# Optimization experiments

Hardware: AMD Instinct MI355X
Metric: run time of the kernel (lower is better)

The kernel has to match this reference:

```python
import jax, jax.numpy as jnp
import numpy as np

D = 1024       # d_model
DR = 1024      # d_rec
FFN = 4096     # ffn_inner
K = 4          # conv_kernel
B, T = 2, 4096
CHUNK = 64
EPS = 1e-6


def setup_inputs() -> dict:
    key = jax.random.key(0)
    ks = jax.random.split(key, 8)
    s = lambda k, shape, scale: jax.random.normal(k, shape, jnp.float32) * scale
    db = np.zeros((DR,), np.float32)
    q = DR // 4
    db[:q] = -2.2
    db[q:3 * q] = 0.0
    db[3 * q:] = 4.6
    return {
        "x": s(ks[0], (B, T, D), 1.0),
        "pre_norm_w": jnp.ones((D,), jnp.float32),
        "conv_w": s(ks[1], (D, 1, K), 0.3),
        "conv_b": jnp.zeros((D,), jnp.float32),
        "w_a": s(ks[2], (DR, D), 0.02),
        "w_i": s(ks[3], (DR, D), 0.02),
        "w_v": s(ks[4], (DR, D), 0.02),
        "out_proj_w": s(ks[5], (D, DR), 0.02),
        "decay_bias": jnp.asarray(db),
        "ffn_norm_w": jnp.ones((D,), jnp.float32),
        "w_gate_up": s(ks[6], (2 * FFN, D), 0.02),
        "w_down": s(ks[7], (D, FFN), 0.02),
    }


def rmsnorm(x, w):
    return x * jax.lax.rsqrt(jnp.mean(x * x, axis=-1, keepdims=True) + EPS) * w


def lin(x, w):  # nn.Linear weight layout (out, in)
    return jnp.einsum('btd,od->bto', x, w)


def causal_conv(h, w, b):
    # depthwise causal conv: h (B,T,D), w (D,1,K)
    hc = jnp.transpose(h, (0, 2, 1))  # (B,D,T)
    out = jax.lax.conv_general_dilated(
        hc, w, window_strides=(1,), padding=[(K - 1, 0)],
        dimension_numbers=('NCH', 'OIH', 'NCH'), feature_group_count=D)
    return jnp.transpose(out, (0, 2, 1)) + b


def chunked_scan(a, v):
    b, s, d = a.shape
    pad = (-s) % CHUNK
    af = jnp.pad(a, ((0, 0), (0, pad), (0, 0)), constant_values=1.0)
    vf = jnp.pad(v, ((0, 0), (0, pad), (0, 0)))
    n = (s + pad) // CHUNK
    dc = af.reshape(b, n, CHUNK, d)
    vc = vf.reshape(b, n, CHUNK, d)
    cum_decay = jnp.exp(jnp.cumsum(jnp.log(jnp.clip(dc, 1e-10)), axis=2))
    intra = cum_decay * jnp.cumsum(vc / jnp.clip(cum_decay, 1e-10), axis=2)

    def step(state, xs):
        cd, it = xs  # (B,CHUNK,d) each
        cs = it + cd * state[:, None, :]
        return cs[:, -1], cs

    _, states = jax.lax.scan(
        step, jnp.zeros((b, d), jnp.float32),
        (jnp.transpose(cum_decay, (1, 0, 2, 3)), jnp.transpose(intra, (1, 0, 2, 3))))
    return jnp.transpose(states, (1, 0, 2, 3)).reshape(b, n * CHUNK, d)[:, :s]


def reference(x, pre_norm_w, conv_w, conv_b, w_a, w_i, w_v, out_proj_w,
              decay_bias, ffn_norm_w, w_gate_up, w_down):
    h = rmsnorm(x, pre_norm_w)
    h = causal_conv(h, conv_w, conv_b)
    a = jax.nn.sigmoid(lin(h, w_a) + decay_bias)
    i_gate = jax.nn.sigmoid(lin(h, w_i))
    v = lin(h, w_v)
    input_signal = jnp.sqrt(jnp.clip(1.0 - a * a, 1e-8)) * (i_gate * v)
    rec_out = chunked_scan(a, input_signal).astype(x.dtype)
    x = x + lin(rec_out, out_proj_w)
    hn = rmsnorm(x, ffn_norm_w)
    gu = lin(hn, w_gate_up)
    gate, up = gu[..., :FFN], gu[..., FFN:]
    x = x + lin(jax.nn.silu(gate) * up, w_down)
    return x
```

## Files before the change

kernel.cpp:

```cpp
#include <hip/hip_runtime.h>

typedef __bf16 bf16_t;
typedef bf16_t bf16x4 __attribute__((ext_vector_type(4)));
typedef bf16_t bf16x8 __attribute__((ext_vector_type(8)));
typedef float f32x4 __attribute__((ext_vector_type(4)));

#define DD 1024
#define TT 4096

__device__ __forceinline__ void gload16(const void* g, void* l) {
    __builtin_amdgcn_global_load_lds(
        (const __attribute__((address_space(1))) void*)g,
        (__attribute__((address_space(3))) void*)l, 16, 0, 0);
}

__global__ __launch_bounds__(256) void cvt_bf16_k(const float* __restrict__ s,
                                                  bf16_t* __restrict__ d, int n) {
    int i = (blockIdx.x * 256 + threadIdx.x) * 4;
    if (i < n) {
        const float4 v = *(const float4*)(s + i);
        bf16x4 o;
        o[0] = (bf16_t)v.x; o[1] = (bf16_t)v.y; o[2] = (bf16_t)v.z; o[3] = (bf16_t)v.w;
        *(bf16x4*)(d + i) = o;
    }
}

__global__ __launch_bounds__(256) void cvt_ileave_k(const float* __restrict__ s0,
                                                    const float* __restrict__ s1,
                                                    bf16_t* __restrict__ d, int total) {
    int i = (blockIdx.x * 256 + threadIdx.x) * 4;
    if (i < total) {
        const int rp = i >> 10, k = i & 1023;
        const int c = rp >> 1;
        const float* src = ((rp & 1) ? s1 : s0) + (long)c * 1024 + k;
        const float4 v = *(const float4*)src;
        bf16x4 o;
        o[0] = (bf16_t)v.x; o[1] = (bf16_t)v.y; o[2] = (bf16_t)v.z; o[3] = (bf16_t)v.w;
        *(bf16x4*)(d + i) = o;
    }
}

__global__ __launch_bounds__(256) void rmsnorm_k(const float* __restrict__ x,
                                                 const float* __restrict__ w,
                                                 bf16_t* __restrict__ ob) {
    const long row = blockIdx.x;
    const float* xr = x + row * DD;
    const int t4 = threadIdx.x * 4;
    float4 v = *(const float4*)(xr + t4);
    float s = v.x*v.x + v.y*v.y + v.z*v.z + v.w*v.w;
    #pragma unroll
    for (int off = 1; off < 64; off <<= 1) s += __shfl_xor(s, off);
    __shared__ float red[4];
    if ((threadIdx.x & 63) == 0) red[threadIdx.x >> 6] = s;
    __syncthreads();
    float tot = red[0] + red[1] + red[2] + red[3];
    float sc = rsqrtf(tot * (1.0f / DD) + 1e-6f);
    float4 wv = *(const float4*)(w + t4);
    bf16x4 o;
    o[0] = (bf16_t)(v.x*sc*wv.x); o[1] = (bf16_t)(v.y*sc*wv.y);
    o[2] = (bf16_t)(v.z*sc*wv.z); o[3] = (bf16_t)(v.w*sc*wv.w);
    *(bf16x4*)(ob + row * DD + t4) = o;
}

__global__ __launch_bounds__(256) void conv_k(const bf16_t* __restrict__ h,
                                              const float* __restrict__ cw,
                                              const float* __restrict__ cb,
                                              bf16_t* __restrict__ hc) {
    const long idx = (long)blockIdx.x * 256 + threadIdx.x;
    const int d = (int)(idx & (DD - 1));
    const long bt = idx >> 10;
    const int t = (int)(bt & (TT - 1));
    const float w0 = cw[d*4+0], w1 = cw[d*4+1], w2 = cw[d*4+2], w3 = cw[d*4+3];
    const bf16_t* hp = h + bt * DD + d;
    float acc = cb[d] + (float)hp[0] * w3;
    if (t >= 1) acc += (float)hp[-DD]     * w2;
    if (t >= 2) acc += (float)hp[-2*DD]   * w1;
    if (t >= 3) acc += (float)hp[-3*DD]   * w0;
    hc[idx] = (bf16_t)acc;
}

__global__ __launch_bounds__(256) void scan1_k(const float* __restrict__ ap,
                                               const float* __restrict__ sp,
                                               float* __restrict__ cd63,
                                               float* __restrict__ i63) {
    const int d = blockIdx.x * 256 + threadIdx.x;
    const int c = blockIdx.y;
    const int b = blockIdx.z;
    const long rowbase = (long)b * TT + (long)c * 64;
    float la = 0.0f, rs = 0.0f, cdv = 0.0f, it = 0.0f;
    for (int t = 0; t < 64; t++) {
        const long off = (rowbase + t) * DD + d;
        const float a = ap[off];
        const float s = sp[off];
        const float sig = sqrtf(fmaxf(1.0f - a * a, 1e-8f)) * s;
        la += __logf(fmaxf(a, 1e-10f));
        cdv = __expf(la);
        rs += sig / fmaxf(cdv, 1e-10f);
        it = cdv * rs;
    }
    const long o = ((long)b * 64 + c) * DD + d;
    cd63[o] = cdv;
    i63[o]  = it;
}

__global__ __launch_bounds__(256) void scan2_k(const float* __restrict__ cd63,
                                               const float* __restrict__ i63,
                                               float* __restrict__ carry_in) {
    const int g = blockIdx.x * 256 + threadIdx.x;
    const int b = g >> 10, d = g & (DD - 1);
    float st = 0.0f;
    for (int c = 0; c < 64; c++) {
        const long o = ((long)b * 64 + c) * DD + d;
        carry_in[o] = st;
        st = i63[o] + cd63[o] * st;
    }
}

__global__ __launch_bounds__(256) void scan3_k(const float* __restrict__ ap,
                                               const float* __restrict__ sp,
                                               const float* __restrict__ carry_in,
                                               bf16_t* __restrict__ rec) {
    const int d = blockIdx.x * 256 + threadIdx.x;
    const int c = blockIdx.y;
    const int b = blockIdx.z;
    const long rowbase = (long)b * TT + (long)c * 64;
    const float carry = carry_in[((long)b * 64 + c) * DD + d];
    float la = 0.0f, rs = 0.0f;
    for (int t = 0; t < 64; t++) {
        const long off = (rowbase + t) * DD + d;
        const float a = ap[off];
        const float s = sp[off];
        const float sig = sqrtf(fmaxf(1.0f - a * a, 1e-8f)) * s;
        la += __logf(fmaxf(a, 1e-10f));
        const float cdv = __expf(la);
        rs += sig / fmaxf(cdv, 1e-10f);
        rec[off] = (bf16_t)(cdv * rs + cdv * carry);
    }
}

enum { EPI_SIGB = 0, EPI_ADDRES = 1, EPI_IV = 2, EPI_GU = 3 };

template<int EPI, int NREP>
__global__ __launch_bounds__(512, 2) void gemm8p_k(const bf16_t* __restrict__ Ag,
                                                   const bf16_t* __restrict__ Bg,
                                                   int M, int N, int K,
                                                   float* outF, bf16_t* outB,
                                                   const float* aux, int ldc) {
    constexpr int BN  = NREP * 64;
    constexpr int ASZ = 16384;
    constexpr int BSZ = BN * 64;
    constexpr int BUF = ASZ + BSZ;
    extern __shared__ bf16_t smem[];
    const int tid = threadIdx.x;
    const int l = tid & 63;
    const int w = tid >> 6;
    const int wm = w >> 2, wn = w & 3;

    const int gx = gridDim.x;
    const int gy = gridDim.y;
    const int lin = blockIdx.y * gx + blockIdx.x;
    long row0, col0;
    if ((gy & 7) == 0) {
        const int rpc = gy >> 3;
        const int q = lin >> 3;
        row0 = (long)((lin & 7) * rpc + q % rpc) * 256;
        col0 = (long)(q / rpc) * (long)BN;
    } else {
        row0 = (long)blockIdx.y * 256;
        col0 = (long)blockIdx.x * BN;
    }

    const int srow = l >> 3;
    const int scol = ((l & 7) ^ srow) * 8;
    const long aBase = row0 + srow;
    const long bBase = col0 + srow;
    const int R0a = w * 32;
    const int R0b = w * (BN / 8);

    const int NT = K >> 6;
    f32x4 acc[8][NREP] = {};

    #pragma unroll
    for (int i = 0; i < NREP; i++)
        gload16(Bg + (bBase + R0b + i * 8) * (long)K + scol, &smem[ASZ + (R0b + i * 8) * 64]);
    #pragma unroll
    for (int i = 0; i < 4; i++)
        gload16(Ag + (aBase + R0a + i * 8) * (long)K + scol, &smem[(R0a + i * 8) * 64]);
    #pragma unroll
    for (int i = 0; i < NREP; i++)
        gload16(Bg + (bBase + R0b + i * 8) * (long)K + 64 + scol, &smem[BUF + ASZ + (R0b + i * 8) * 64]);

    const int lq = (l >> 4) * 8;
    const int rA = wm * 128 + (l & 15);
    const int rB = wn * (NREP * 16) + (l & 15);

    for (int t = 0; t < NT; t++) {
        const int cb = (t & 1) * BUF;
        const int ob = BUF - cb;
        const long kg1 = (long)(t + 1) * 64 + scol;
        const long kg2 = (long)(t + 2) * 64 + scol;
        bf16x8 Bf[2][NREP], Af[4];

        if (t + 1 < NT) {
            gload16(Ag + (aBase + R0a) * (long)K + kg1, &smem[ob + R0a * 64]);
            gload16(Ag + (aBase + R0a + 8) * (long)K + kg1, &smem[ob + (R0a + 8) * 64]);
        }
        if (t == NT - 1)            { asm volatile("s_waitcnt vmcnt(0)" ::: "memory"); }
        else if constexpr (NREP == 4) { asm volatile("s_waitcnt vmcnt(6)" ::: "memory"); }
        else                        { asm volatile("s_waitcnt vmcnt(4)" ::: "memory"); }
        asm volatile("s_barrier" ::: "memory");
        #pragma unroll
        for (int n = 0; n < NREP; n++) {
            const int r = rB + n * 16;
            Bf[0][n] = *(const bf16x8*)&smem[cb + ASZ + r * 64 + (((lq * 2) ^ ((r & 7) << 4)) >> 1)];
        }
        #pragma unroll
        for (int m = 0; m < 4; m++) {
            const int r = rA + m * 16;
            Af[m] = *(const bf16x8*)&smem[cb + r * 64 + (((lq * 2) ^ ((r & 7) << 4)) >> 1)];
        }
        __builtin_amdgcn_s_setprio(1);
        #pragma unroll
        for (int m = 0; m < 4; m++)
            #pragma unroll
            for (int n = 0; n < NREP; n++)
                acc[m][n] = __builtin_amdgcn_mfma_f32_16x16x32_bf16(Af[m], Bf[0][n], acc[m][n], 0, 0, 0);
        __builtin_amdgcn_s_setprio(0);
        asm volatile("s_barrier" ::: "memory");

        #pragma unroll
        for (int m = 0; m < 4; m++) {
            const int r = rA + 64 + m * 16;
            Af[m] = *(const bf16x8*)&smem[cb + r * 64 + (((lq * 2) ^ ((r & 7) << 4)) >> 1)];
        }
        #pragma unroll
        for (int n = 0; n < NREP; n++) {
            const int r = rB + n * 16;
            Bf[1][n] = *(const bf16x8*)&smem[cb + ASZ + r * 64 + ((((lq * 2) ^ ((r & 7) << 4)) ^ 64) >> 1)];
        }
        if (t + 1 < NT) {
            gload16(Ag + (aBase + R0a + 16) * (long)K + kg1, &smem[ob + (R0a + 16) * 64]);
            gload16(Ag + (aBase + R0a + 24) * (long)K + kg1, &smem[ob + (R0a + 24) * 64]);
        }
        asm volatile("s_barrier" ::: "memory");
        __builtin_amdgcn_s_setprio(1);
        #pragma unroll
        for (int m = 0; m < 4; m++)
            #pragma unroll
            for (int n = 0; n < NREP; n++)
                acc[m + 4][n] = __builtin_amdgcn_mfma_f32_16x16x32_bf16(Af[m], Bf[0][n], acc[m + 4][n], 0, 0, 0);
        __builtin_amdgcn_s_setprio(0);
        asm volatile("s_barrier" ::: "memory");

        #pragma unroll
        for (int m = 0; m < 4; m++) {
            const int r = rA + m * 16;
            Af[m] = *(const bf16x8*)&smem[cb + r * 64 + ((((lq + 32) * 2) ^ ((r & 7) << 4)) >> 1)];
        }
        if (t + 2 < NT) {
            gload16(Bg + (bBase + R0b) * (long)K + kg2, &smem[cb + ASZ + R0b * 64]);
            if constexpr (NREP == 4)
                gload16(Bg + (bBase + R0b + 8) * (long)K + kg2, &smem[cb + ASZ + (R0b + 8) * 64]);
        }
        asm volatile("s_barrier" ::: "memory");
        __builtin_amdgcn_s_setprio(1);
        #pragma unroll
        for (int m = 0; m < 4; m++)
            #pragma unroll
            for (int n = 0; n < NREP; n++)
                acc[m][n] = __builtin_amdgcn_mfma_f32_16x16x32_bf16(Af[m], Bf[1][n], acc[m][n], 0, 0, 0);
        __builtin_amdgcn_s_setprio(0);
        asm volatile("s_barrier" ::: "memory");

        #pragma unroll
        for (int m = 0; m < 4; m++) {
            const int r = rA + 64 + m * 16;
            Af[m] = *(const bf16x8*)&smem[cb + r * 64 + ((((lq + 32) * 2) ^ ((r & 7) << 4)) >> 1)];
        }
        if (t + 2 < NT) {
            if constexpr (NREP == 4) {
                gload16(Bg + (bBase + R0b + 16) * (long)K + kg2, &smem[cb + ASZ + (R0b + 16) * 64]);
                gload16(Bg + (bBase + R0b + 24) * (long)K + kg2, &smem[cb + ASZ + (R0b + 24) * 64]);
            } else {
                gload16(Bg + (bBase + R0b + 8) * (long)K + kg2, &smem[cb + ASZ + (R0b + 8) * 64]);
            }
        }
        asm volatile("s_barrier" ::: "memory");
        __builtin_amdgcn_s_setprio(1);
        #pragma unroll
        for (int m = 0; m < 4; m++)
            #pragma unroll
            for (int n = 0; n < NREP; n++)
                acc[m + 4][n] = __builtin_amdgcn_mfma_f32_16x16x32_bf16(Af[m], Bf[1][n], acc[m + 4][n], 0, 0, 0);
        __builtin_amdgcn_s_setprio(0);
        asm volatile("s_barrier" ::: "memory");
    }

    #pragma unroll
    for (int m = 0; m < 8; m++) {
        const long r0 = row0 + wm * 128 + m * 16 + (l >> 4) * 4;
        #pragma unroll
        for (int n = 0; n < NREP; n++) {
            const long cc = col0 + wn * (NREP * 16) + n * 16 + (l & 15);
            f32x4 v = acc[m][n];
            #pragma unroll
            for (int j = 0; j < 4; j++) {
                const long r = r0 + j;
                const float xv = v[j];
                if (EPI == EPI_SIGB) {
                    outF[r * ldc + cc] = 1.0f / (1.0f + __expf(-(xv + aux[cc])));
                } else if (EPI == EPI_ADDRES) {
                    outF[r * ldc + cc] = xv + aux[r * ldc + cc];
                } else if (EPI == EPI_IV) {
                    const float px = __shfl_xor(xv, 1);
                    if ((l & 1) == 0)
                        outF[r * ldc + (cc >> 1)] = px / (1.0f + __expf(-xv));
                } else {
                    const float px = __shfl_xor(xv, 1);
                    if ((l & 1) == 0)
                        outB[r * ldc + (cc >> 1)] = (bf16_t)(xv / (1.0f + __expf(-xv)) * px);
                }
            }
        }
    }
}

extern "C" void kernel_launch(void* const* d_in, const int* in_sizes, int n_in,
                              void* d_out, int out_size, void* d_ws, size_t ws_size,
                              hipStream_t stream) {
    const float* x   = (const float*)d_in[0];
    const float* pnw = (const float*)d_in[1];
    const float* cw  = (const float*)d_in[2];
    const float* cb  = (const float*)d_in[3];
    const float* wa  = (const float*)d_in[4];
    const float* wi  = (const float*)d_in[5];
    const float* wv  = (const float*)d_in[6];
    const float* wop = (const float*)d_in[7];
    const float* db  = (const float*)d_in[8];
    const float* fnw = (const float*)d_in[9];
    const float* wgu = (const float*)d_in[10];
    const float* wdn = (const float*)d_in[11];
    float* out = (float*)d_out;

    char* ws = (char*)d_ws;
    bf16_t* wab   = (bf16_t*)(ws + 0);
    bf16_t* wivb  = (bf16_t*)(ws + 2097152);
    bf16_t* wopb  = (bf16_t*)(ws + 6291456);
    bf16_t* wgub  = (bf16_t*)(ws + 8388608);
    bf16_t* wdnb  = (bf16_t*)(ws + 25165824);
    bf16_t* hb    = (bf16_t*)(ws + 33554432);
    bf16_t* hn    = hb;
    bf16_t* hc    = (bf16_t*)(ws + 50331648);
    bf16_t* rec   = hc;
    float*  a_p   = (float*)(ws + 67108864);
    float*  s_p   = (float*)(ws + 100663296);
    bf16_t* act   = (bf16_t*)(ws + 67108864);
    float*  cd63  = (float*)(ws + 134217728);
    float*  i63   = (float*)(ws + 134742016);
    float*  carry = (float*)(ws + 135266304);

    const int LDS4 = 131072;
    const int LDS2 = 98304;
    hipFuncSetAttribute((const void*)gemm8p_k<EPI_SIGB, 2>,   hipFuncAttributeMaxDynamicSharedMemorySize, LDS2);
    hipFuncSetAttribute((const void*)gemm8p_k<EPI_IV, 4>,     hipFuncAttributeMaxDynamicSharedMemorySize, LDS4);
    hipFuncSetAttribute((const void*)gemm8p_k<EPI_ADDRES, 2>, hipFuncAttributeMaxDynamicSharedMemorySize, LDS2);
    hipFuncSetAttribute((const void*)gemm8p_k<EPI_GU, 4>,     hipFuncAttributeMaxDynamicSharedMemorySize, LDS4);

    cvt_bf16_k  <<<1024, 256, 0, stream>>>(wa,  wab,  1048576);
    cvt_ileave_k<<<2048, 256, 0, stream>>>(wi,  wv, wivb, 2097152);
    cvt_bf16_k  <<<1024, 256, 0, stream>>>(wop, wopb, 1048576);
    cvt_ileave_k<<<8192, 256, 0, stream>>>(wgu, wgu + 4194304, wgub, 8388608);
    cvt_bf16_k  <<<4096, 256, 0, stream>>>(wdn, wdnb, 4194304);

    rmsnorm_k<<<8192, 256, 0, stream>>>(x, pnw, hb);
    conv_k<<<32768, 256, 0, stream>>>(hb, cw, cb, hc);

    gemm8p_k<EPI_SIGB, 2><<<dim3(8, 32), 512, LDS2, stream>>>(hc, wab,  8192, 1024, 1024,
                                                              a_p, nullptr, db, 1024);
    gemm8p_k<EPI_IV, 4>  <<<dim3(8, 32), 512, LDS4, stream>>>(hc, wivb, 8192, 2048, 1024,
                                                              s_p, nullptr, nullptr, 1024);
    scan1_k<<<dim3(4, 64, 2), 256, 0, stream>>>(a_p, s_p, cd63, i63);
    scan2_k<<<8, 256, 0, stream>>>(cd63, i63, carry);
    scan3_k<<<dim3(4, 64, 2), 256, 0, stream>>>(a_p, s_p, carry, rec);

    gemm8p_k<EPI_ADDRES, 2><<<dim3(8, 32), 512, LDS2, stream>>>(rec, wopb, 8192, 1024, 1024,
                                                                out, nullptr, x, 1024);
    rmsnorm_k<<<8192, 256, 0, stream>>>(out, fnw, hn);
    gemm8p_k<EPI_GU, 4><<<dim3(32, 32), 512, LDS4, stream>>>(hn, wgub, 8192, 8192, 1024,
                                                             nullptr, act, nullptr, 4096);
    gemm8p_k<EPI_ADDRES, 2><<<dim3(8, 32), 512, LDS2, stream>>>(act, wdnb, 8192, 1024, 4096,
                                                                out, nullptr, out, 1024);
}
```

Baseline: 480.8 us.

## Restructure GEMM main loop into two-phase schedule with full-tile prefetch

Replaces the eight-phase GEMM inner loop, which interleaved partial global-to-LDS loads with four MFMA groups and many barriers, with a two-phase loop. Each iteration issues whole next-next tile loads at once, preloads the A and B fragments for both k-halves into registers, and uses two barriers per iteration instead of eight. The aim is to cut barrier and synchronisation overhead and give longer uninterrupted MFMA runs. The cost is higher register pressure from holding more fragments, and bursty global-load issue that may hide latency less well.

After: 468.8 us. 1.03x faster.

```diff
diff --git a/kernel.cpp b/kernel.cpp
--- a/kernel.cpp
+++ b/kernel.cpp
@@ -141,7 +141,7 @@
 enum { EPI_SIGB = 0, EPI_ADDRES = 1, EPI_IV = 2, EPI_GU = 3 };
 
 template<int EPI, int NREP>
-__global__ __launch_bounds__(512, 2) void gemm8p_k(const bf16_t* __restrict__ Ag,
+__global__ __launch_bounds__(512, 2) void gemm2p_k(const bf16_t* __restrict__ Ag,
                                                    const bf16_t* __restrict__ Bg,
                                                    int M, int N, int K,
                                                    float* outF, bf16_t* outB,
@@ -180,121 +180,98 @@
     const int NT = K >> 6;
     f32x4 acc[8][NREP] = {};
 
-    #pragma unroll
-    for (int i = 0; i < NREP; i++)
-        gload16(Bg + (bBase + R0b + i * 8) * (long)K + scol, &smem[ASZ + (R0b + i * 8) * 64]);
-    #pragma unroll
-    for (int i = 0; i < 4; i++)
-        gload16(Ag + (aBase + R0a + i * 8) * (long)K + scol, &smem[(R0a + i * 8) * 64]);
-    #pragma unroll
-    for (int i = 0; i < NREP; i++)
-        gload16(Bg + (bBase + R0b + i * 8) * (long)K + 64 + scol, &smem[BUF + ASZ + (R0b + i * 8) * 64]);
-
-    const int lq = (l >> 4) * 8;
+    const int lq2 = (l >> 4) * 16;
     const int rA = wm * 128 + (l & 15);
     const int rB = wn * (NREP * 16) + (l & 15);
+    const int eA0 = rA * 64 + ((lq2 ^ ((rA & 7) << 4)) >> 1);
+    const int eB0 = ASZ + rB * 64 + ((lq2 ^ ((rB & 7) << 4)) >> 1);
+
+    #define STAGE_A(tt, off)                                                          \
+        { const long kgk = (long)(tt) * 64 + scol;                                    \
+          _Pragma("unroll")                                                           \
+          for (int i = 0; i < 4; i++)                                                 \
+              gload16(Ag + (aBase + R0a + i * 8) * (long)K + kgk,                     \
+                      &smem[(off) + (R0a + i * 8) * 64]); }
+    #define STAGE_B(tt, off)                                                          \
+        { const long kgk = (long)(tt) * 64 + scol;                                    \
+          _Pragma("unroll")                                                           \
+          for (int i = 0; i < NREP; i++)                                              \
+              gload16(Bg + (bBase + R0b + i * 8) * (long)K + kgk,                     \
+                      &smem[(off) + ASZ + (R0b + i * 8) * 64]); }
+
+    STAGE_A(0, 0); STAGE_B(0, 0);
+    STAGE_A(1, BUF); STAGE_B(1, BUF);
+    if constexpr (NREP == 4) { asm volatile("s_waitcnt vmcnt(8)" ::: "memory"); }
+    else                     { asm volatile("s_waitcnt vmcnt(6)" ::: "memory"); }
+    asm volatile("s_barrier" ::: "memory");
+
+    bf16x8 pA[2][4], pB[2][NREP];
+    #pragma unroll
+    for (int kk = 0; kk < 2; kk++) {
+        const int xo = kk * 32;
+        #pragma unroll
+        for (int n = 0; n < NREP; n++)
+            pB[kk][n] = *(const bf16x8*)&smem[(eB0 ^ xo) + n * 1024];
+        #pragma unroll
+        for (int m = 0; m < 4; m++)
+            pA[kk][m] = *(const bf16x8*)&smem[(eA0 ^ xo) + m * 1024];
+    }
 
     for (int t = 0; t < NT; t++) {
-        const int cb = (t & 1) * BUF;
-        const int ob = BUF - cb;
-        const long kg1 = (long)(t + 1) * 64 + scol;
-        const long kg2 = (long)(t + 2) * 64 + scol;
-        bf16x8 Bf[2][NREP], Af[4];
-
-        if (t + 1 < NT) {
-            gload16(Ag + (aBase + R0a) * (long)K + kg1, &smem[ob + R0a * 64]);
-            gload16(Ag + (aBase + R0a + 8) * (long)K + kg1, &smem[ob + (R0a + 8) * 64]);
-        }
-        if (t == NT - 1)            { asm volatile("s_waitcnt vmcnt(0)" ::: "memory"); }
-        else if constexpr (NREP == 4) { asm volatile("s_waitcnt vmcnt(6)" ::: "memory"); }
-        else                        { asm volatile("s_waitcnt vmcnt(4)" ::: "memory"); }
-        asm volatile("s_barrier" ::: "memory");
-        #pragma unroll
-        for (int n = 0; n < NREP; n++) {
-            const int r = rB + n * 16;
-            Bf[0][n] = *(const bf16x8*)&smem[cb + ASZ + r * 64 + (((lq * 2) ^ ((r & 7) << 4)) >> 1)];
-        }
-        #pragma unroll
-        for (int m = 0; m < 4; m++) {
-            const int r = rA + m * 16;
-            Af[m] = *(const bf16x8*)&smem[cb + r * 64 + (((lq * 2) ^ ((r & 7) << 4)) >> 1)];
-        }
+        const int co = (t & 1) ? BUF : 0;
+        const int oo = BUF - co;
+        bf16x8 a1[2][4];
+
         __builtin_amdgcn_s_setprio(1);
         #pragma unroll
-        for (int m = 0; m < 4; m++)
-            #pragma unroll
-            for (int n = 0; n < NREP; n++)
-                acc[m][n] = __builtin_amdgcn_mfma_f32_16x16x32_bf16(Af[m], Bf[0][n], acc[m][n], 0, 0, 0);
+        for (int kk = 0; kk < 2; kk++)
+            #pragma unroll
+            for (int m = 0; m < 4; m++)
+                #pragma unroll
+                for (int n = 0; n < NREP; n++)
+                    acc[m][n] = __builtin_amdgcn_mfma_f32_16x16x32_bf16(pA[kk][m], pB[kk][n], acc[m][n], 0, 0, 0);
         __builtin_amdgcn_s_setprio(0);
-        asm volatile("s_barrier" ::: "memory");
-
-        #pragma unroll
-        for (int m = 0; m < 4; m++) {
-            const int r = rA + 64 + m * 16;
-            Af[m] = *(const bf16x8*)&smem[cb + r * 64 + (((lq * 2) ^ ((r & 7) << 4)) >> 1)];
-        }
-        #pragma unroll
-        for (int n = 0; n < NREP; n++) {
-            const int r = rB + n * 16;
-            Bf[1][n] = *(const bf16x8*)&smem[cb + ASZ + r * 64 + ((((lq * 2) ^ ((r & 7) << 4)) ^ 64) >> 1)];
-        }
-        if (t + 1 < NT) {
-            gload16(Ag + (aBase + R0a + 16) * (long)K + kg1, &smem[ob + (R0a + 16) * 64]);
-            gload16(Ag + (aBase + R0a + 24) * (long)K + kg1, &smem[ob + (R0a + 24) * 64]);
+        #pragma unroll
+        for (int kk = 0; kk < 2; kk++) {
+            const int xo = kk * 32;
+            #pragma unroll
+            for (int m = 0; m < 4; m++)
+                a1[kk][m] = *(const bf16x8*)&smem[co + (eA0 ^ xo) + 4096 + m * 1024];
         }
         asm volatile("s_barrier" ::: "memory");
+
+        if (t + 2 < NT) { STAGE_A(t + 2, co); STAGE_B(t + 2, co); }
         __builtin_amdgcn_s_setprio(1);
         #pragma unroll
-        for (int m = 0; m < 4; m++)
-            #pragma unroll
-            for (int n = 0; n < NREP; n++)
-                acc[m + 4][n] = __builtin_amdgcn_mfma_f32_16x16x32_bf16(Af[m], Bf[0][n], acc[m + 4][n], 0, 0, 0);
+        for (int kk = 0; kk < 2; kk++)
+            #pragma unroll
+            for (int m = 0; m < 4; m++)
+                #pragma unroll
+                for (int n = 0; n < NREP; n++)
+                    acc[m + 4][n] = __builtin_amdgcn_mfma_f32_16x16x32_bf16(a1[kk][m], pB[kk][n], acc[m + 4][n], 0, 0, 0);
         __builtin_amdgcn_s_setprio(0);
-        asm volatile("s_barrier" ::: "memory");
-
-        #pragma unroll
-        for (int m = 0; m < 4; m++) {
-            const int r = rA + m * 16;
-            Af[m] = *(const bf16x8*)&smem[cb + r * 64 + ((((lq + 32) * 2) ^ ((r & 7) << 4)) >> 1)];
-        }
         if (t + 2 < NT) {
-            gload16(Bg + (bBase + R0b) * (long)K + kg2, &smem[cb + ASZ + R0b * 64]);
-            if constexpr (NREP == 4)
-                gload16(Bg + (bBase + R0b + 8) * (long)K + kg2, &smem[cb + ASZ + (R0b + 8) * 64]);
+            if constexpr (NREP == 4) { asm volatile("s_waitcnt vmcnt(8)" ::: "memory"); }
+            else                     { asm volatile("s_waitcnt vmcnt(6)" ::: "memory"); }
+        } else if (t + 1 < NT) {
+            asm volatile("s_waitcnt vmcnt(0)" ::: "memory");
         }
         asm volatile("s_barrier" ::: "memory");
-        __builtin_amdgcn_s_setprio(1);
-        #pragma unroll
-        for (int m = 0; m < 4; m++)
-            #pragma unroll
-            for (int n = 0; n < NREP; n++)
-                acc[m][n] = __builtin_amdgcn_mfma_f32_16x16x32_bf16(Af[m], Bf[1][n], acc[m][n], 0, 0, 0);
-        __builtin_amdgcn_s_setprio(0);
-        asm volatile("s_barrier" ::: "memory");
-
-        #pragma unroll
-        for (int m = 0; m < 4; m++) {
-            const int r = rA + 64 + m * 16;
-            Af[m] = *(const bf16x8*)&smem[cb + r * 64 + ((((lq + 32) * 2) ^ ((r & 7) << 4)) >> 1)];
-        }
-        if (t + 2 < NT) {
-            if constexpr (NREP == 4) {
-                gload16(Bg + (bBase + R0b + 16) * (long)K + kg2, &smem[cb + ASZ + (R0b + 16) * 64]);
-                gload16(Bg + (bBase + R0b + 24) * (long)K + kg2, &smem[cb + ASZ + (R0b + 24) * 64]);
-            } else {
-                gload16(Bg + (bBase + R0b + 8) * (long)K + kg2, &smem[cb + ASZ + (R0b + 8) * 64]);
+        if (t + 1 < NT) {
+            #pragma unroll
+            for (int kk = 0; kk < 2; kk++) {
+                const int xo = kk * 32;
+                #pragma unroll
+                for (int n = 0; n < NREP; n++)
+                    pB[kk][n] = *(const bf16x8*)&smem[oo + (eB0 ^ xo) + n * 1024];
+                #pragma unroll
+                for (int m = 0; m < 4; m++)
+                    pA[kk][m] = *(const bf16x8*)&smem[oo + (eA0 ^ xo) + m * 1024];
             }
         }
-        asm volatile("s_barrier" ::: "memory");
-        __builtin_amdgcn_s_setprio(1);
-        #pragma unroll
-        for (int m = 0; m < 4; m++)
-            #pragma unroll
-            for (int n = 0; n < NREP; n++)
-                acc[m + 4][n] = __builtin_amdgcn_mfma_f32_16x16x32_bf16(Af[m], Bf[1][n], acc[m + 4][n], 0, 0, 0);
-        __builtin_amdgcn_s_setprio(0);
-        asm volatile("s_barrier" ::: "memory");
-    }
+    }
+    #undef STAGE_A
+    #undef STAGE_B
 
     #pragma unroll
     for (int m = 0; m < 8; m++) {
@@ -361,10 +338,10 @@
 
     const int LDS4 = 131072;
     const int LDS2 = 98304;
-    hipFuncSetAttribute((const void*)gemm8p_k<EPI_SIGB, 2>,   hipFuncAttributeMaxDynamicSharedMemorySize, LDS2);
-    hipFuncSetAttribute((const void*)gemm8p_k<EPI_IV, 4>,     hipFuncAttributeMaxDynamicSharedMemorySize, LDS4);
-    hipFuncSetAttribute((const void*)gemm8p_k<EPI_ADDRES, 2>, hipFuncAttributeMaxDynamicSharedMemorySize, LDS2);
-    hipFuncSetAttribute((const void*)gemm8p_k<EPI_GU, 4>,     hipFuncAttributeMaxDynamicSharedMemorySize, LDS4);
+    hipFuncSetAttribute((const void*)gemm2p_k<EPI_SIGB, 2>,   hipFuncAttributeMaxDynamicSharedMemorySize, LDS2);
+    hipFuncSetAttribute((const void*)gemm2p_k<EPI_IV, 4>,     hipFuncAttributeMaxDynamicSharedMemorySize, LDS4);
+    hipFuncSetAttribute((const void*)gemm2p_k<EPI_ADDRES, 2>, hipFuncAttributeMaxDynamicSharedMemorySize, LDS2);
+    hipFuncSetAttribute((const void*)gemm2p_k<EPI_GU, 4>,     hipFuncAttributeMaxDynamicSharedMemorySize, LDS4);
 
     cvt_bf16_k  <<<1024, 256, 0, stream>>>(wa,  wab,  1048576);
     cvt_ileave_k<<<2048, 256, 0, stream>>>(wi,  wv, wivb, 2097152);
@@ -375,19 +352,19 @@
     rmsnorm_k<<<8192, 256, 0, stream>>>(x, pnw, hb);
     conv_k<<<32768, 256, 0, stream>>>(hb, cw, cb, hc);
 
-    gemm8p_k<EPI_SIGB, 2><<<dim3(8, 32), 512, LDS2, stream>>>(hc, wab,  8192, 1024, 1024,
+    gemm2p_k<EPI_SIGB, 2><<<dim3(8, 32), 512, LDS2, stream>>>(hc, wab,  8192, 1024, 1024,
                                                               a_p, nullptr, db, 1024);
-    gemm8p_k<EPI_IV, 4>  <<<dim3(8, 32), 512, LDS4, stream>>>(hc, wivb, 8192, 2048, 1024,
+    gemm2p_k<EPI_IV, 4>  <<<dim3(8, 32), 512, LDS4, stream>>>(hc, wivb, 8192, 2048, 1024,
                                                               s_p, nullptr, nullptr, 1024);
     scan1_k<<<dim3(4, 64, 2), 256, 0, stream>>>(a_p, s_p, cd63, i63);
     scan2_k<<<8, 256, 0, stream>>>(cd63, i63, carry);
     scan3_k<<<dim3(4, 64, 2), 256, 0, stream>>>(a_p, s_p, carry, rec);
 
-    gemm8p_k<EPI_ADDRES, 2><<<dim3(8, 32), 512, LDS2, stream>>>(rec, wopb, 8192, 1024, 1024,
+    gemm2p_k<EPI_ADDRES, 2><<<dim3(8, 32), 512, LDS2, stream>>>(rec, wopb, 8192, 1024, 1024,
                                                                 out, nullptr, x, 1024);
     rmsnorm_k<<<8192, 256, 0, stream>>>(out, fnw, hn);
-    gemm8p_k<EPI_GU, 4><<<dim3(32, 32), 512, LDS4, stream>>>(hn, wgub, 8192, 8192, 1024,
+    gemm2p_k<EPI_GU, 4><<<dim3(32, 32), 512, LDS4, stream>>>(hn, wgub, 8192, 8192, 1024,
                                                              nullptr, act, nullptr, 4096);
-    gemm8p_k<EPI_ADDRES, 2><<<dim3(8, 32), 512, LDS2, stream>>>(act, wdnb, 8192, 1024, 4096,
+    gemm2p_k<EPI_ADDRES, 2><<<dim3(8, 32), 512, LDS2, stream>>>(act, wdnb, 8192, 1024, 4096,
                                                                 out, nullptr, out, 1024);
 }
```
